# Performance work log

Measured on AMD Instinct MI355X. Metric: run time of the kernel, lower is better.

## Reference

```python
import jax, jax.numpy as jnp
import numpy as np

NEG_INF = -jnp.inf


def setup_inputs() -> dict:
    key = jax.random.key(0)
    k1, k2, k3, k4 = jax.random.split(key, 4)
    B, V = 256, 128000
    logits = jax.random.normal(k1, (B, V), dtype=jnp.float32)
    temperatures = jax.random.uniform(k2, (B,), dtype=jnp.float32, minval=0.5, maxval=1.5)
    top_ks = jax.random.randint(k3, (B,), 0, 1024, dtype=jnp.int32)
    top_ps = jax.random.uniform(k4, (B,), dtype=jnp.float32)
    return {"logits": logits, "temperatures": temperatures, "top_ks": top_ks, "top_ps": top_ps}


def _filtered_logits(logits, temperatures, top_ks, top_ps):
    # Faithful vectorized version of the per-row torch loops.
    B, V = logits.shape
    x = logits.astype(jnp.float32) / temperatures[:, None]

    # Sort each row descending once; reuse for top-k and top-p.
    order = jnp.argsort(-x, axis=-1)                       # [B, V] desc indices
    sorted_x = jnp.take_along_axis(x, order, axis=-1)      # [B, V]
    ranks = jnp.arange(V)[None, :]                         # [1, V]

    # top-k: active only when 0 < k < V (matches torch branch)
    k = top_ks[:, None].astype(jnp.int32)
    topk_active = (k > 0) & (k < V)
    keep_k = jnp.where(topk_active, ranks < k, True)
    sorted_x = jnp.where(keep_k, sorted_x, NEG_INF)

    # top-p on softmax of top-k-filtered logits. Softmax is order-preserving,
    # so sorted probs == softmax of sorted (filtered) logits.
    sorted_probs = jax.nn.softmax(sorted_x, axis=-1)
    cumsum = jnp.cumsum(sorted_probs, axis=-1)
    p = top_ps[:, None]
    cutoff = jnp.sum(cumsum <= p, axis=-1, keepdims=True)  # (cumsum<=p).sum()
    cutoff = jnp.where(cutoff < V, cutoff + 1, cutoff)     # include next token
    topp_active = (p > 0.0) & (p < 1.0)
    keep_p = jnp.where(topp_active, ranks < cutoff, True)
    sorted_x = jnp.where(keep_p, sorted_x, NEG_INF)

    # Unsort back to original token order.
    inv = jnp.argsort(order, axis=-1)
    return jnp.take_along_axis(sorted_x, inv, axis=-1)


def reference(logits, temperatures, top_ks, top_ps):
    x = _filtered_logits(logits, temperatures, top_ks, top_ps)
    probs = jax.nn.softmax(x, axis=-1)
    # Gumbel-max style sampling: argmax(probs / Exp(1)) (torch .exponential_ trick)
    e = jax.random.exponential(jax.random.key(42), probs.shape, dtype=jnp.float32)
    e = jnp.maximum(e, 1e-10)
    return jnp.argmax(probs / e, axis=-1)
```

## Files before the change

kernel.cpp:

```cpp
#include <hip/hip_runtime.h>
#include <stdint.h>

#define VV 128000
#define BLOCK 1024
#define NB 4096
#define CAP 4096

typedef unsigned long long ull;

__device__ __forceinline__ uint32_t rotl32(uint32_t x, int r){ return (x << r) | (x >> (32 - r)); }

__device__ __forceinline__ float exp_noise(uint32_t f){
  const uint32_t ks0 = 0u, ks1 = 42u, ks2 = 0x1BD11BDAu ^ 0u ^ 42u;
  uint32_t x0 = 0u + ks0;
  uint32_t x1 = f + ks1;
#define R1(r) { x0 += x1; x1 = rotl32(x1, r); x1 ^= x0; }
  R1(13) R1(15) R1(26) R1(6)   x0 += ks1; x1 += ks2 + 1u;
  R1(17) R1(29) R1(16) R1(24)  x0 += ks2; x1 += ks0 + 2u;
  R1(13) R1(15) R1(26) R1(6)   x0 += ks0; x1 += ks1 + 3u;
  R1(17) R1(29) R1(16) R1(24)  x0 += ks1; x1 += ks2 + 4u;
  R1(13) R1(15) R1(26) R1(6)   x0 += ks2; x1 += ks0 + 5u;
#undef R1
  uint32_t bits = x0 ^ x1;
  float u = __uint_as_float((bits >> 9) | 0x3F800000u) - 1.0f;
  float e = -log1pf(-u);
  return fmaxf(e, 1e-10f);
}

__device__ __forceinline__ uint32_t fkey(float x){
  uint32_t u = __float_as_uint(x);
  return u ^ ((u & 0x80000000u) ? 0xFFFFFFFFu : 0x80000000u);
}
__device__ __forceinline__ float keyval(uint32_t k){
  uint32_t bits = (k & 0x80000000u) ? (k ^ 0x80000000u) : ~k;
  return __uint_as_float(bits);
}

__device__ void suffix_scan_u(uint32_t* h, uint32_t* tmp, int tid){
  const int base = tid * 4;
  uint32_t l0=h[base], l1=h[base+1], l2=h[base+2], l3=h[base+3];
  uint32_t s3=l3, s2=l2+s3, s1=l1+s2, s0=l0+s1;
  tmp[tid] = s0; __syncthreads();
  for (int d=1; d<BLOCK; d<<=1){
    uint32_t add = (tid+d<BLOCK) ? tmp[tid+d] : 0u;
    __syncthreads();
    tmp[tid] += add;
    __syncthreads();
  }
  uint32_t E = (tid+1<BLOCK) ? tmp[tid+1] : 0u;
  h[base]=s0+E; h[base+1]=s1+E; h[base+2]=s2+E; h[base+3]=s3+E;
  __syncthreads();
}
__device__ void suffix_scan_f(float* h, float* tmp, int tid){
  const int base = tid * 4;
  float l0=h[base], l1=h[base+1], l2=h[base+2], l3=h[base+3];
  float s3=l3, s2=l2+s3, s1=l1+s2, s0=l0+s1;
  tmp[tid] = s0; __syncthreads();
  for (int d=1; d<BLOCK; d<<=1){
    float add = (tid+d<BLOCK) ? tmp[tid+d] : 0.f;
    __syncthreads();
    tmp[tid] += add;
    __syncthreads();
  }
  float E = (tid+1<BLOCK) ? tmp[tid+1] : 0.f;
  h[base]=s0+E; h[base+1]=s1+E; h[base+2]=s2+E; h[base+3]=s3+E;
  __syncthreads();
}

__device__ uint32_t select_tth_smallest(uint32_t* a, int n, int t){
  for (int i=0;i<t;i++){
    int mi=i; uint32_t mv=a[i];
    for (int j=i+1;j<n;j++) if (a[j]<mv){ mv=a[j]; mi=j; }
    a[mi]=a[i]; a[i]=mv;
  }
  return a[t-1];
}

#define ROW4_BEGIN \
    for (int c0 = tid; c0 < VV/4; c0 += BLOCK*4){ \
      float4 qv[4]; int cb[4]; bool gv[4]; \
      _Pragma("unroll") \
      for (int t=0;t<4;t++){ int cc = c0 + t*BLOCK; gv[t] = (cc < VV/4); cb[t] = cc*4; if (gv[t]) qv[t] = rp[cc]; } \
      _Pragma("unroll") \
      for (int t=0;t<4;t++) if (gv[t]){ \
        float xs[4] = {qv[t].x, qv[t].y, qv[t].z, qv[t].w}; \
        _Pragma("unroll") \
        for (int j=0;j<4;j++){ \
          float x = xs[j]/T; \
          uint32_t u = fkey(x); \
          uint32_t idx = (uint32_t)(cb[t]+j); \
          (void)idx;
#define ROW4_END } } }

__global__ __launch_bounds__(BLOCK) void sampler_kernel(
    const float* __restrict__ logits, const float* __restrict__ temps,
    const int* __restrict__ topks, const float* __restrict__ topps,
    int* __restrict__ out)
{
  __shared__ uint32_t wu[NB];
  __shared__ ull      cand[CAP];
  __shared__ float    tmpf[BLOCK];
  __shared__ uint32_t tmpu[BLOCK];
  __shared__ float    ck[BLOCK];
  __shared__ ull      red[BLOCK];
  __shared__ int s_idx, s_n, s_tk, s_ntk, s_tp, s_ntp, s_cnt;
  __shared__ uint32_t s_uk, s_idxk, s_up, s_idxp;
  __shared__ float s_m, s_Zk, s_Ztot;

  float* S  = (float*)cand;
  float* wf = ((float*)cand) + NB;

  const int b   = blockIdx.x;
  const int tid = threadIdx.x;
  const float T = temps[b];
  const int   k = topks[b];
  const float p = topps[b];
  const float* row = logits + (size_t)b * VV;
  const float4* rp = reinterpret_cast<const float4*>(row);
  const bool topk_act = (k > 0) && (k < VV);
  const bool topp_act = (p > 0.0f) && (p < 1.0f);

  if (topk_act){
    for (int i=tid;i<NB;i+=BLOCK) wu[i]=0u;
    __syncthreads();
    ROW4_BEGIN
      atomicAdd(&wu[u>>20], 1u);
    ROW4_END
    __syncthreads();
    suffix_scan_u(wu, tmpu, tid);
    if (tid==0) s_idx = 0;
    __syncthreads();
    for (int i=tid;i<NB;i+=BLOCK){
      uint32_t a  = wu[i];
      uint32_t nn = (i+1<NB) ? wu[i+1] : 0u;
      if (a >= (uint32_t)k && nn < (uint32_t)k) s_idx = i;
    }
    __syncthreads();
    const uint32_t beta = (uint32_t)s_idx;
    const int n = (int)wu[beta];
    if (n <= CAP){
      if (tid==0) s_n = 0;
      __syncthreads();
      ROW4_BEGIN
        if ((u>>20) >= beta){
          int pos = atomicAdd(&s_n, 1);
          cand[pos] = (((ull)(~u))<<32) | idx;
        }
      ROW4_END
      __syncthreads();
      int N = 2; while (N < n) N <<= 1;
      for (int i=tid;i<N;i+=BLOCK) if (i >= n) cand[i] = 0xFFFFFFFFFFFFFFFFull;
      __syncthreads();
      for (int len=2; len<=N; len<<=1){
        for (int j=len>>1; j>0; j>>=1){
          for (int i=tid; i<N; i+=BLOCK){
            int l = i ^ j;
            if (l > i){
              ull a = cand[i], c2 = cand[l];
              bool asc = ((i & len) == 0);
              if (asc ? (a > c2) : (a < c2)){ cand[i]=c2; cand[l]=a; }
            }
          }
          __syncthreads();
        }
      }
      const int kk = k;
      const float m = keyval(~(uint32_t)(cand[0]>>32));
      float w = 0.f; uint32_t myidx = 0u;
      if (tid < kk){
        ull e = cand[tid];
        myidx = (uint32_t)e;
        w = expf(keyval(~(uint32_t)(e>>32)) - m);
      }
      ck[tid] = w; __syncthreads();
      for (int d=BLOCK/2; d>0; d>>=1){
        if (tid < d) ck[tid] += ck[tid+d];
        __syncthreads();
      }
      if (tid==0) s_Ztot = ck[0];
      __syncthreads();
      const float Zk = s_Ztot;
      ck[tid] = w / Zk; __syncthreads();
      for (int d=1; d<BLOCK; d<<=1){
        float add = (tid >= d) ? ck[tid-d] : 0.f;
        __syncthreads();
        ck[tid] += add;
        __syncthreads();
      }
      if (tid==0) s_cnt = 0;
      tmpu[tid] = (tid < kk && ck[tid] <= p) ? 1u : 0u;
      __syncthreads();
      for (int d=BLOCK/2; d>0; d>>=1){
        if (tid < d) tmpu[tid] += tmpu[tid+d];
        __syncthreads();
      }
      int L;
      if (!topp_act) L = kk;
      else { int c = (int)tmpu[0]; L = (c >= kk) ? kk : (c + 1); }
      ull best = 0ull;
      if (tid < L){
        float q = w / exp_noise((uint32_t)b * (uint32_t)VV + myidx);
        best = (((ull)__float_as_uint(q)) << 32) | (uint32_t)(~myidx);
      }
      red[tid] = best; __syncthreads();
      for (int d=BLOCK/2; d>0; d>>=1){
        if (tid < d){ ull o = red[tid+d]; if (o > red[tid]) red[tid] = o; }
        __syncthreads();
      }
      if (tid==0) out[b] = (int)(~(uint32_t)(red[0] & 0xFFFFFFFFull));
      return;
    }
    __syncthreads();
  }

  for (int i=tid;i<NB;i+=BLOCK){ S[i]=0.f; wu[i]=0u; }
  __syncthreads();
  float lmax = -3.4e38f;
  ROW4_BEGIN
    lmax = fmaxf(lmax, x);
    atomicAdd(&wu[u>>20], 1u);
    atomicAdd(&S[u>>20], expf(x));
  ROW4_END
  tmpf[tid] = lmax; __syncthreads();
  for (int d=BLOCK/2; d>0; d>>=1){
    if (tid < d) tmpf[tid] = fmaxf(tmpf[tid], tmpf[tid+d]);
    __syncthreads();
  }
  if (tid==0) s_m = tmpf[0];
  __syncthreads();
  suffix_scan_u(wu, tmpu, tid);
  suffix_scan_f(S,  tmpf, tid);

  uint32_t uk = 0u, idxk = 0xFFFFFFFFu;
  int bk1 = -1;
  if (topk_act){
    if (tid==0) s_idx = 0;
    __syncthreads();
    for (int i=tid;i<NB;i+=BLOCK){
      uint32_t a  = wu[i];
      uint32_t nn = (i+1<NB) ? wu[i+1] : 0u;
      if (a >= (uint32_t)k && nn < (uint32_t)k) s_idx = i;
    }
    __syncthreads();
    bk1 = s_idx;
    const uint32_t c_above1 = (bk1+1<NB) ? wu[bk1+1] : 0u;
    const float    M_above1 = (bk1+1<NB) ? S[bk1+1]  : 0.f;
    __syncthreads();
    for (int i=tid;i<NB;i+=BLOCK){ wu[i]=0u; wf[i]=0.f; }
    __syncthreads();
    ROW4_BEGIN
      if ((int)(u>>20) == bk1){
        atomicAdd(&wu[(u>>8)&0xFFFu], 1u);
        atomicAdd(&wf[(u>>8)&0xFFFu], expf(x));
      }
    ROW4_END
    __syncthreads();
    suffix_scan_u(wu, tmpu, tid);
    suffix_scan_f(wf, tmpf, tid);
    if (tid==0) s_idx = 0;
    __syncthreads();
    for (int i=tid;i<NB;i+=BLOCK){
      uint32_t a  = c_above1 + wu[i];
      uint32_t nn = c_above1 + ((i+1<NB) ? wu[i+1] : 0u);
      if (a >= (uint32_t)k && nn < (uint32_t)k) s_idx = i;
    }
    __syncthreads();
    const int bk2 = s_idx;
    const uint32_t c_above2 = c_above1 + ((bk2+1<NB) ? wu[bk2+1] : 0u);
    const float    M_above2 = M_above1 + ((bk2+1<NB) ? wf[bk2+1] : 0.f);
    __syncthreads();
    if (tid < 256){ wu[tid]=0u; wf[tid]=0.f; }
    __syncthreads();
    const uint32_t top24k = (((uint32_t)bk1)<<12) | (uint32_t)bk2;
    ROW4_BEGIN
      if ((u>>8) == top24k){
        atomicAdd(&wu[u & 0xFFu], 1u);
        atomicAdd(&wf[u & 0xFFu], expf(x));
      }
    ROW4_END
    __syncthreads();
    if (tid==0){
      uint32_t r = 0u; float mr = 0.f; int b3 = 0;
      for (int i=255;i>=0;--i){
        if (c_above2 + r + wu[i] >= (uint32_t)k){ b3 = i; break; }
        r += wu[i]; mr += wf[i];
      }
      const uint32_t cgt = c_above2 + r;
      const float mgt = M_above2 + mr;
      const int nt = (int)wu[b3];
      const int tk = k - (int)cgt;
      s_uk  = (((uint32_t)bk1)<<20) | (((uint32_t)bk2)<<8) | (uint32_t)b3;
      s_tk  = tk; s_ntk = nt;
      s_Zk  = mgt + (float)tk * expf(keyval(s_uk));
      s_n   = 0;
    }
    __syncthreads();
    uk = s_uk;
    if (s_tk < s_ntk){
      ROW4_BEGIN
        if (u == uk){
          int pos = atomicAdd(&s_n, 1);
          if (pos < NB) wu[pos] = idx;
        }
      ROW4_END
      __syncthreads();
      if (tid==0){
        int n2 = min(s_n, NB);
        int t  = min(s_tk, n2);
        s_idxk = select_tth_smallest(wu, n2, t);
      }
      __syncthreads();
      idxk = s_idxk;
    }
  }
  const float Zk = topk_act ? s_Zk : S[0];

  uint32_t up = 0u, idxp = 0xFFFFFFFFu;
  const float tgt = p * Zk;
  const bool pall = (!topp_act) || (tgt >= Zk);
  if (!pall){
    if (tid==0) s_idx = -2;
    __syncthreads();
    for (int i=tid;i<NB;i+=BLOCK){
      if (i > bk1){
        float a  = S[i];
        float nn = (i+1<NB) ? S[i+1] : 0.f;
        if (a > tgt && nn <= tgt) s_idx = i;
      }
    }
    __syncthreads();
    int bp1 = (s_idx >= 0) ? s_idx : bk1;
    if (bp1 < 0) bp1 = 0;
    const float Mab = (bp1+1<NB) ? S[bp1+1] : 0.f;
    __syncthreads();
    for (int i=tid;i<NB;i+=BLOCK) wf[i]=0.f;
    __syncthreads();
    ROW4_BEGIN
      if ((int)(u>>20) == bp1){
        bool kk_ok = (!topk_act) || (u > uk) || (u == uk && idx <= idxk);
        if (kk_ok) atomicAdd(&wf[(u>>8)&0xFFFu], expf(x));
      }
    ROW4_END
    __syncthreads();
    suffix_scan_f(wf, tmpf, tid);
    if (tid==0) s_idx = -2;
    __syncthreads();
    for (int i=tid;i<NB;i+=BLOCK){
      float a  = Mab + wf[i];
      float nn = Mab + ((i+1<NB) ? wf[i+1] : 0.f);
      if (a > tgt && nn <= tgt) s_idx = i;
    }
    __syncthreads();
    int bp2;
    if (s_idx >= 0){ bp2 = s_idx; }
    else {
      if (tid==0) s_idx = NB;
      __syncthreads();
      for (int i=tid;i<NB;i+=BLOCK){
        float a  = wf[i];
        float nn = (i+1<NB) ? wf[i+1] : 0.f;
        if (a > nn) atomicMin(&s_idx, i);
      }
      __syncthreads();
      bp2 = (s_idx < NB) ? s_idx : 0;
    }
    const float Mab2 = Mab + ((bp2+1<NB) ? wf[bp2+1] : 0.f);
    __syncthreads();
    if (tid < 256){ wf[tid]=0.f; wu[tid]=0u; }
    __syncthreads();
    const uint32_t top24p = (((uint32_t)bp1)<<12) | (uint32_t)bp2;
    ROW4_BEGIN
      if ((u>>8) == top24p){
        bool kk_ok = (!topk_act) || (u > uk) || (u == uk && idx <= idxk);
        if (kk_ok){
          atomicAdd(&wf[u & 0xFFu], expf(x));
          atomicAdd(&wu[u & 0xFFu], 1u);
        }
      }
    ROW4_END
    __syncthreads();
    if (tid==0){
      float run = 0.f; int b3 = -1; float mgt = 0.f;
      for (int i=255;i>=0;--i){
        float sufn = run; run += wf[i];
        if (Mab2 + run > tgt && Mab2 + sufn <= tgt){ b3 = i; mgt = Mab2 + sufn; break; }
      }
      if (b3 < 0){
        float run2 = 0.f;
        for (int i=255;i>=0;--i){
          if (wu[i] > 0u){ b3 = i; mgt = Mab2 + run2; }
          run2 += wf[i];
        }
        if (b3 < 0){ b3 = 0; mgt = Mab2; }
      }
      const uint32_t upv = (((uint32_t)bp1)<<20) | (((uint32_t)bp2)<<8) | (uint32_t)b3;
      const int ntp = (int)wu[b3];
      const float ev = expf(keyval(upv));
      int t = 0;
      for (int j=1;j<=ntp;j++){
        float before = mgt + (float)(j-1) * ev;
        if (before / Zk <= p) t++; else break;
      }
      if (t < 1) t = 1;
      s_up = upv; s_tp = t; s_ntp = ntp; s_n = 0;
    }
    __syncthreads();
    up = s_up;
    if (s_tp < s_ntp){
      ROW4_BEGIN
        if (u == up){
          bool kk_ok = (!topk_act) || (u > uk) || (u == uk && idx <= idxk);
          if (kk_ok){
            int pos = atomicAdd(&s_n, 1);
            if (pos < NB) wu[pos] = idx;
          }
        }
      ROW4_END
      __syncthreads();
      if (tid==0){
        int n2 = min(s_n, NB);
        int t  = min(s_tp, n2);
        s_idxp = select_tth_smallest(wu, n2, t);
      }
      __syncthreads();
      idxp = s_idxp;
    }
  }

  const float m  = s_m;
  const float Zs = Zk * expf(-m);
  ull best = 0ull;
  ROW4_BEGIN
    bool kk_ok = (!topk_act) || (u > uk) || (u == uk && idx <= idxk);
    bool kp_ok = pall || (u > up) || (u == up && idx <= idxp);
    if (kk_ok && kp_ok){
      float q = (expf(x - m) / Zs) / exp_noise((uint32_t)b * (uint32_t)VV + idx);
      ull pk = (((ull)__float_as_uint(q)) << 32) | (uint32_t)(~idx);
      best = (pk > best) ? pk : best;
    }
  ROW4_END
  red[tid] = best; __syncthreads();
  for (int d=BLOCK/2; d>0; d>>=1){
    if (tid < d){ ull o = red[tid+d]; if (o > red[tid]) red[tid] = o; }
    __syncthreads();
  }
  if (tid==0) out[b] = (int)(~(uint32_t)(red[0] & 0xFFFFFFFFull));
}

extern "C" void kernel_launch(void* const* d_in, const int* in_sizes, int n_in,
                              void* d_out, int out_size, void* d_ws, size_t ws_size,
                              hipStream_t stream) {
  (void)in_sizes; (void)n_in; (void)out_size; (void)d_ws; (void)ws_size;
  const float* logits = (const float*)d_in[0];
  const float* temps  = (const float*)d_in[1];
  const int*   ks     = (const int*)d_in[2];
  const float* ps     = (const float*)d_in[3];
  int* out = (int*)d_out;
  sampler_kernel<<<256, BLOCK, 0, stream>>>(logits, temps, ks, ps, out);
}
```

Baseline: 247.3 us.

## Refine top-k candidates with second-level radix histogram and skip temperature division

The histogram pass now keys on raw logits instead of logits divided by temperature, relying on positive temperatures preserving order, and divides by T only for the k selected values. The histogram is split into four sub-copies indexed by tid&3 to reduce shared-memory atomic contention. When more than 1024 candidates survive the first 12-bit bucket pass, a second 12-bit histogram pass narrows them to at most 1024 before the bitonic sort, shrinking the sort. Shared memory is consolidated into one 100 KB aliased buffer, which may lower occupancy, and the extra histogram passes add synchronisation.

```diff
diff --git a/kernel.cpp b/kernel.cpp
--- a/kernel.cpp
+++ b/kernel.cpp
@@ -76,6 +76,37 @@
   return a[t-1];
 }
 
+__device__ void bitonic_sort(ull* a, int N, int tid){
+  for (int len=2; len<=N; len<<=1){
+    for (int j=len>>1; j>0; j>>=1){
+      for (int i=tid; i<N; i+=BLOCK){
+        int l = i ^ j;
+        if (l > i){
+          ull x = a[i], y = a[l];
+          bool asc = ((i & len) == 0);
+          if (asc ? (x > y) : (x < y)){ a[i]=y; a[l]=x; }
+        }
+      }
+      __syncthreads();
+    }
+  }
+}
+
+#define ROW4R_BEGIN \
+    for (int c0 = tid; c0 < VV/4; c0 += BLOCK*4){ \
+      float4 qv[4]; int cb[4]; bool gv[4]; \
+      _Pragma("unroll") \
+      for (int t=0;t<4;t++){ int cc = c0 + t*BLOCK; gv[t] = (cc < VV/4); cb[t] = cc*4; if (gv[t]) qv[t] = rp[cc]; } \
+      _Pragma("unroll") \
+      for (int t=0;t<4;t++) if (gv[t]){ \
+        float vs[4] = {qv[t].x, qv[t].y, qv[t].z, qv[t].w}; \
+        _Pragma("unroll") \
+        for (int j=0;j<4;j++){ \
+          uint32_t u = fkey(vs[j]); \
+          uint32_t idx = (uint32_t)(cb[t]+j); \
+          (void)idx;
+#define ROW4R_END } } }
+
 #define ROW4_BEGIN \
     for (int c0 = tid; c0 < VV/4; c0 += BLOCK*4){ \
       float4 qv[4]; int cb[4]; bool gv[4]; \
@@ -97,18 +128,22 @@
     const int* __restrict__ topks, const float* __restrict__ topps,
     int* __restrict__ out)
 {
-  __shared__ uint32_t wu[NB];
-  __shared__ ull      cand[CAP];
-  __shared__ float    tmpf[BLOCK];
-  __shared__ uint32_t tmpu[BLOCK];
-  __shared__ float    ck[BLOCK];
-  __shared__ ull      red[BLOCK];
-  __shared__ int s_idx, s_n, s_tk, s_ntk, s_tp, s_ntp, s_cnt;
+  __shared__ __align__(16) uint8_t SM[102400];
+  uint32_t* h4    = (uint32_t*)SM;
+  ull*      cand  = (ull*)SM;
+  uint32_t* h2    = (uint32_t*)(SM + 32*1024);
+  ull*      sort2 = (ull*)(SM + 48*1024);
+  float*    S     = (float*)SM;
+  float*    wf    = (float*)(SM + 16*1024);
+  uint32_t* wu    = (uint32_t*)(SM + 64*1024);
+  float*    tmpf  = (float*)(SM + 80*1024);
+  uint32_t* tmpu  = (uint32_t*)(SM + 84*1024);
+  float*    ck    = (float*)(SM + 88*1024);
+  ull*      red   = (ull*)(SM + 92*1024);
+
+  __shared__ int s_idx, s_n, s_n2, s_tk, s_ntk, s_tp, s_ntp;
   __shared__ uint32_t s_uk, s_idxk, s_up, s_idxp;
   __shared__ float s_m, s_Zk, s_Ztot;
-
-  float* S  = (float*)cand;
-  float* wf = ((float*)cand) + NB;
 
   const int b   = blockIdx.x;
   const int tid = threadIdx.x;
@@ -121,11 +156,14 @@
   const bool topp_act = (p > 0.0f) && (p < 1.0f);
 
   if (topk_act){
-    for (int i=tid;i<NB;i+=BLOCK) wu[i]=0u;
-    __syncthreads();
-    ROW4_BEGIN
-      atomicAdd(&wu[u>>20], 1u);
-    ROW4_END
+    for (int i=tid;i<4*NB;i+=BLOCK) h4[i]=0u;
+    __syncthreads();
+    ROW4R_BEGIN
+      atomicAdd(&h4[((u>>20)<<2) | (uint32_t)(tid&3)], 1u);
+    ROW4R_END
+    __syncthreads();
+    for (int i=tid;i<NB;i+=BLOCK)
+      wu[i] = h4[(i<<2)] + h4[(i<<2)|1] + h4[(i<<2)|2] + h4[(i<<2)|3];
     __syncthreads();
     suffix_scan_u(wu, tmpu, tid);
     if (tid==0) s_idx = 0;
@@ -138,39 +176,67 @@
     __syncthreads();
     const uint32_t beta = (uint32_t)s_idx;
     const int n = (int)wu[beta];
+    const uint32_t c_above = (beta+1<NB) ? wu[beta+1] : 0u;
     if (n <= CAP){
       if (tid==0) s_n = 0;
       __syncthreads();
-      ROW4_BEGIN
+      ROW4R_BEGIN
         if ((u>>20) >= beta){
           int pos = atomicAdd(&s_n, 1);
           cand[pos] = (((ull)(~u))<<32) | idx;
         }
-      ROW4_END
-      __syncthreads();
-      int N = 2; while (N < n) N <<= 1;
-      for (int i=tid;i<N;i+=BLOCK) if (i >= n) cand[i] = 0xFFFFFFFFFFFFFFFFull;
-      __syncthreads();
-      for (int len=2; len<=N; len<<=1){
-        for (int j=len>>1; j>0; j>>=1){
-          for (int i=tid; i<N; i+=BLOCK){
-            int l = i ^ j;
-            if (l > i){
-              ull a = cand[i], c2 = cand[l];
-              bool asc = ((i & len) == 0);
-              if (asc ? (a > c2) : (a < c2)){ cand[i]=c2; cand[l]=a; }
+      ROW4R_END
+      __syncthreads();
+      ull* srt; int m;
+      if (n <= 1024){ srt = cand; m = n; }
+      else {
+        for (int i=tid;i<NB;i+=BLOCK) h2[i]=0u;
+        __syncthreads();
+        for (int i=tid;i<n;i+=BLOCK){
+          uint32_t u2 = ~(uint32_t)(cand[i]>>32);
+          if ((u2>>20) == beta) atomicAdd(&h2[(u2>>8)&0xFFFu], 1u);
+        }
+        __syncthreads();
+        suffix_scan_u(h2, tmpu, tid);
+        const uint32_t kr = (uint32_t)k - c_above;
+        if (tid==0) s_idx = 0;
+        __syncthreads();
+        for (int i=tid;i<NB;i+=BLOCK){
+          uint32_t a  = h2[i];
+          uint32_t nn = (i+1<NB) ? h2[i+1] : 0u;
+          if (a >= kr && nn < kr) s_idx = i;
+        }
+        __syncthreads();
+        const uint32_t gam = (uint32_t)s_idx;
+        const int np = (int)(c_above + h2[gam]);
+        if (np <= 1024){
+          if (tid==0) s_n2 = 0;
+          __syncthreads();
+          const uint32_t cut24 = (beta<<12) | gam;
+          for (int i=tid;i<n;i+=BLOCK){
+            ull e = cand[i];
+            uint32_t u2 = ~(uint32_t)(e>>32);
+            if ((u2>>8) >= cut24){
+              int pos = atomicAdd(&s_n2, 1);
+              sort2[pos] = e;
             }
           }
           __syncthreads();
-        }
-      }
+          srt = sort2; m = np;
+        } else { srt = cand; m = n; }
+      }
+      int N = 2; while (N < m) N <<= 1;
+      for (int i=tid;i<N;i+=BLOCK) if (i >= m) srt[i] = 0xFFFFFFFFFFFFFFFFull;
+      __syncthreads();
+      bitonic_sort(srt, N, tid);
       const int kk = k;
-      const float m = keyval(~(uint32_t)(cand[0]>>32));
+      const float xm = keyval(~(uint32_t)(srt[0]>>32)) / T;
       float w = 0.f; uint32_t myidx = 0u;
       if (tid < kk){
-        ull e = cand[tid];
+        ull e = srt[tid];
         myidx = (uint32_t)e;
-        w = expf(keyval(~(uint32_t)(e>>32)) - m);
+        float xv = keyval(~(uint32_t)(e>>32)) / T;
+        w = expf(xv - xm);
       }
       ck[tid] = w; __syncthreads();
       for (int d=BLOCK/2; d>0; d>>=1){
@@ -187,7 +253,6 @@
         ck[tid] += add;
         __syncthreads();
       }
-      if (tid==0) s_cnt = 0;
       tmpu[tid] = (tid < kk && ck[tid] <= p) ? 1u : 0u;
       __syncthreads();
       for (int d=BLOCK/2; d>0; d>>=1){
```

Result: faster. 231.5 us (-6.4%).
